# Performance work log

Hardware: AMD Instinct MI355X
Metric: run time of the kernel (lower is better)

The kernel has to match this reference:

```python
import jax, jax.numpy as jnp
import numpy as np

B, S, D, H = 4, 2048, 1024, 16
HD = D // H


def setup_inputs() -> dict:
    key = jax.random.key(0)
    ks = jax.random.split(key, 5)
    scale = 1.0 / np.sqrt(D)
    return {
        "x": jax.random.normal(ks[0], (B, S, D), dtype=jnp.float32),
        "W_q": jax.random.normal(ks[1], (D, D), dtype=jnp.float32) * scale,
        "W_k": jax.random.normal(ks[2], (D, D), dtype=jnp.float32) * scale,
        "W_v": jax.random.normal(ks[3], (D, D), dtype=jnp.float32) * scale,
        "W_o": jax.random.normal(ks[4], (D, D), dtype=jnp.float32) * scale,
    }


def reference(x, W_q, W_k, W_v, W_o):
    b, s, d = x.shape
    # fused QKV projections; reshape to per-head layout [b, s, H, HD]
    q = (x @ W_q).reshape(b, s, H, HD)
    k = (x @ W_k).reshape(b, s, H, HD)
    v = (x @ W_v).reshape(b, s, H, HD)
    # scaled dot-product scores [b, H, s, s]
    scores = jnp.einsum("bqhd,bkhd->bhqk", q, k) / jnp.sqrt(jnp.asarray(HD, x.dtype))
    # causal mask: disallow attending to future positions (j > i)
    causal = jnp.tril(jnp.ones((s, s), dtype=bool))
    scores = jnp.where(causal[None, None], scores, jnp.finfo(x.dtype).min)
    attn = jax.nn.softmax(scores, axis=-1)
    # attention output back to [b, s, d], then output projection (W_o applied as x @ W_o.T)
    out = jnp.einsum("bhqk,bkhd->bqhd", attn, v).reshape(b, s, d)
    return out @ W_o.T
```

## Files before the change

### kernel.cpp

```cpp
#include <hip/hip_runtime.h>
#include <hip/hip_bf16.h>
#include <stdint.h>

#define B_  4
#define S_  2048
#define D_  1024
#define H_  16
#define HD_ 64
#define M_  (B_*S_)

typedef __bf16 bf16_t;
typedef __bf16 bf16x8 __attribute__((ext_vector_type(8)));
typedef __bf16 bf16x4 __attribute__((ext_vector_type(4)));
typedef __bf16 bf16x2 __attribute__((ext_vector_type(2)));
typedef float  f32x4  __attribute__((ext_vector_type(4)));
typedef unsigned int uint2v __attribute__((ext_vector_type(2)));

#define EXP2(x) __builtin_amdgcn_exp2f(x)
#define CS_ 0.18033688011112042f

__global__ void cvt_f32_to_bf16(const float* __restrict__ src, bf16_t* __restrict__ dst, int n) {
  int stride = gridDim.x * blockDim.x * 4;
  for (int i = (blockIdx.x * blockDim.x + threadIdx.x) * 4; i < n; i += stride) {
    float4 v = *(const float4*)(src + i);
    bf16x4 o = { (bf16_t)v.x, (bf16_t)v.y, (bf16_t)v.z, (bf16_t)v.w };
    *(bf16x4*)(dst + i) = o;
  }
}

__global__ void cvt_transpose_w(const float* __restrict__ wq, const float* __restrict__ wk,
                                const float* __restrict__ wv, const float* __restrict__ wof,
                                bf16_t* __restrict__ dst, bf16_t* __restrict__ wob) {
  __shared__ float t[32][33];
  int w = blockIdx.z;
  int c0 = blockIdx.x * 32, r0 = blockIdx.y * 32;
  int tx = threadIdx.x, ty = threadIdx.y;
  if (w == 3) {
#pragma unroll
    for (int i = 0; i < 4; i++)
      wob[(size_t)(r0 + ty + i * 8) * D_ + c0 + tx] =
          (bf16_t)wof[(size_t)(r0 + ty + i * 8) * D_ + c0 + tx];
    return;
  }
  const float* src = (w == 0) ? wq : (w == 1) ? wk : wv;
  const float scl = (w == 0) ? CS_ : 1.0f;
#pragma unroll
  for (int i = 0; i < 4; i++)
    t[ty + i * 8][tx] = src[(size_t)(r0 + ty + i * 8) * D_ + c0 + tx];
  __syncthreads();
#pragma unroll
  for (int i = 0; i < 4; i++)
    dst[(size_t)(w * D_ + c0 + ty + i * 8) * D_ + r0 + tx] = (bf16_t)(t[tx][ty + i * 8] * scl);
}

template <typename OutT>
__global__ void gemm_nt(const bf16_t* __restrict__ A, const bf16_t* __restrict__ Bt,
                        OutT* __restrict__ C, int Mt, int N, int K) {
  __shared__ bf16_t As[128 * 64];
  __shared__ bf16_t Bs[128 * 64];
  const int bn = blockIdx.x, bm = blockIdx.y;
  const int tid = threadIdx.x;
  const int wv = tid >> 6, lane = tid & 63;
  const int wr = wv >> 1, wc = wv & 1;
  const int g = lane >> 4, r16 = lane & 15;
  const int m0 = bm * 128, n0 = bn * 128;

  f32x4 acc[4][4] = {};

  for (int kt = 0; kt < K; kt += 64) {
#pragma unroll
    for (int c = 0; c < 4; c++) {
      int ch = wv * 4 + c;
      int o = ch * 1024 + lane * 16;
      int row = o >> 7;
      int c16 = (o >> 4) & 7;
      const bf16_t* gA = A + (size_t)(m0 + row) * K + kt + ((c16 ^ (row & 7)) * 8);
      __builtin_amdgcn_global_load_lds((const __attribute__((address_space(1))) void*)gA,
          (__attribute__((address_space(3))) void*)((char*)As + ch * 1024), 16, 0, 0);
    }
#pragma unroll
    for (int c = 0; c < 4; c++) {
      int ch = wv * 4 + c;
      int o = ch * 1024 + lane * 16;
      int row = o >> 7;
      int c16 = (o >> 4) & 7;
      const bf16_t* gB = Bt + (size_t)(n0 + row) * K + kt + ((c16 ^ (row & 7)) * 8);
      __builtin_amdgcn_global_load_lds((const __attribute__((address_space(1))) void*)gB,
          (__attribute__((address_space(3))) void*)((char*)Bs + ch * 1024), 16, 0, 0);
    }
    __syncthreads();

#pragma unroll
    for (int kk = 0; kk < 2; kk++) {
      bf16x8 af[4], bfv[4];
#pragma unroll
      for (int i = 0; i < 4; i++) {
        int row = wr * 64 + i * 16 + r16;
        af[i] = *(const bf16x8*)((char*)As + row * 128 + (((kk * 4 + g) ^ (row & 7)) * 16));
      }
#pragma unroll
      for (int j = 0; j < 4; j++) {
        int row = wc * 64 + j * 16 + r16;
        bfv[j] = *(const bf16x8*)((char*)Bs + row * 128 + (((kk * 4 + g) ^ (row & 7)) * 16));
      }
#pragma unroll
      for (int i = 0; i < 4; i++)
#pragma unroll
        for (int j = 0; j < 4; j++)
          acc[i][j] = __builtin_amdgcn_mfma_f32_16x16x32_bf16(af[i], bfv[j], acc[i][j], 0, 0, 0);
    }
    __syncthreads();
  }

#pragma unroll
  for (int i = 0; i < 4; i++)
#pragma unroll
    for (int j = 0; j < 4; j++)
#pragma unroll
      for (int rr = 0; rr < 4; rr++) {
        int grow = m0 + wr * 64 + i * 16 + g * 4 + rr;
        int gcol = n0 + wc * 64 + j * 16 + r16;
        C[(size_t)grow * N + gcol] = (OutT)acc[i][j][rr];
      }
}

__global__ __launch_bounds__(256, 3) void attn_kernel(const bf16_t* __restrict__ QKV,
                                                      bf16_t* __restrict__ AO) {
  const int bh = blockIdx.x;
  const int qt = 31 - (int)blockIdx.y;
  const int b = bh >> 4, h = bh & 15;
  const int tid = threadIdx.x, wv = tid >> 6, lane = tid & 63;
  const int g = lane >> 4, r16 = lane & 15;

  __shared__ bf16_t Ks[2][64 * 64];
  __shared__ bf16_t Vt[2][64 * 64];

  const size_t rowbase = (size_t)b * S_;
  const bf16_t* Qg = QKV + (rowbase + qt * 64) * 3072 + h * HD_;
  const bf16_t* Kg = QKV + rowbase * 3072 + 1024 + h * HD_;
  const bf16_t* Vg = QKV + rowbase * 3072 + 2048 + h * HD_;

  bf16x8 qf0, qf1;
  {
    int row = wv * 16 + r16;
    const bf16_t* p = Qg + (size_t)row * 3072;
    qf0 = *(const bf16x8*)(p + g * 8);
    qf1 = *(const bf16x8*)(p + 32 + g * 8);
  }

  f32x4 o_acc[4] = {};
  float lrow = 0.f;
  const int base_row = qt * 64 + wv * 16;

  const int kp0 = tid >> 4, dq = tid & 15;
  bf16x4 va0, vb0, va1, vb1;

  auto issueK = [&](int t, int buf) {
    const int kv0 = t * 64;
#pragma unroll
    for (int c = 0; c < 2; c++) {
      int chunkid = wv * 2 + c;
      int o = chunkid * 1024 + lane * 16;
      int row = o >> 7;
      int ch = (o >> 4) & 7;
      const bf16_t* src = Kg + (size_t)(kv0 + row) * 3072 + ((ch ^ (row & 7)) * 8);
      __builtin_amdgcn_global_load_lds((const __attribute__((address_space(1))) void*)src,
          (__attribute__((address_space(3))) void*)((char*)(&Ks[buf][0]) + chunkid * 1024), 16, 0, 0);
    }
  };
  auto loadV = [&](int t) {
    const int kv0 = t * 64;
    const bf16_t* p0 = Vg + (size_t)(kv0 + kp0 * 2) * 3072 + dq * 4;
    va0 = *(const bf16x4*)p0;
    vb0 = *(const bf16x4*)(p0 + 3072);
    const bf16_t* p1 = Vg + (size_t)(kv0 + (16 + kp0) * 2) * 3072 + dq * 4;
    va1 = *(const bf16x4*)p1;
    vb1 = *(const bf16x4*)(p1 + 3072);
  };
  auto writeV = [&](int buf) {
#pragma unroll
    for (int j = 0; j < 4; j++) {
      int d = dq * 4 + j;
      int sz = (((d & 7) ^ (d >> 3)) << 2);
      bf16x2 q0 = { va0[j], vb0[j] };
      *(bf16x2*)(&Vt[buf][d * 64 + (kp0 ^ sz) * 2]) = q0;
      bf16x2 q1 = { va1[j], vb1[j] };
      *(bf16x2*)(&Vt[buf][d * 64 + ((16 + kp0) ^ sz) * 2]) = q1;
    }
  };

  issueK(0, 0);
  loadV(0);

  const int ntiles = qt + 1;
  for (int t = 0; t < ntiles; t++) {
    const int cur = t & 1;
    const int kv0 = t * 64;

    asm volatile("s_waitcnt vmcnt(0)" ::: "memory");
    writeV(cur);
    __syncthreads();
    if (t + 1 < ntiles) { issueK(t + 1, cur ^ 1); loadV(t + 1); }

    const bool skip = kv0 > base_row + 15;
    const bool needmask = (kv0 + 63) > base_row;

    f32x4 st[4];
    if (!skip) {
      __builtin_amdgcn_s_setprio(1);
#pragma unroll
      for (int sub = 0; sub < 4; sub++) {
        int krow = sub * 16 + r16;
        bf16x8 k0 = *(const bf16x8*)((char*)(&Ks[cur][0]) + krow * 128 + ((g ^ (krow & 7)) * 16));
        bf16x8 k1 = *(const bf16x8*)((char*)(&Ks[cur][0]) + krow * 128 + (((4 + g) ^ (krow & 7)) * 16));
        if (kv0 + sub * 16 > base_row + 15) {
          f32x4 ninf = { -1e30f, -1e30f, -1e30f, -1e30f };
          st[sub] = ninf;
          continue;
        }
        f32x4 z = {};
        z = __builtin_amdgcn_mfma_f32_16x16x32_bf16(k0, qf0, z, 0, 0, 0);
        z = __builtin_amdgcn_mfma_f32_16x16x32_bf16(k1, qf1, z, 0, 0, 0);
        st[sub] = z;
      }
      __builtin_amdgcn_s_setprio(0);

      const int qrow = base_row + r16;
      if (needmask) {
#pragma unroll
        for (int sub = 0; sub < 4; sub++)
#pragma unroll
          for (int rr = 0; rr < 4; rr++)
            if (kv0 + sub * 16 + g * 4 + rr > qrow) st[sub][rr] = -1e30f;
      }
      float lsum = 0.f;
      unsigned int W[4][2];
#pragma unroll
      for (int sub = 0; sub < 4; sub++)
#pragma unroll
        for (int rrp = 0; rrp < 2; rrp++) {
          float p0 = EXP2(st[sub][2 * rrp]);
          float p1 = EXP2(st[sub][2 * rrp + 1]);
          lsum += p0 + p1;
          bf16x2 pp = { (bf16_t)p0, (bf16_t)p1 };
          W[sub][rrp] = *(unsigned int*)&pp;
        }
      lrow += lsum;
      unsigned int pfw[2][4];
#pragma unroll
      for (int k2 = 0; k2 < 2; k2++)
#pragma unroll
        for (int rrp = 0; rrp < 2; rrp++) {
          uint2v xy = __builtin_amdgcn_permlane32_swap(W[2 * k2][rrp], W[2 * k2 + 1][rrp],
                                                       false, false);
          uint2v zw = __builtin_amdgcn_permlane16_swap(xy[0], xy[1], false, false);
          pfw[k2][rrp]     = zw[0];
          pfw[k2][2 + rrp] = zw[1];
        }
      bf16x8 pf[2];
#pragma unroll
      for (int kh = 0; kh < 2; kh++) {
        union { unsigned int u[4]; bf16x8 v8; } U;
        U.u[0] = pfw[kh][0]; U.u[1] = pfw[kh][1];
        U.u[2] = pfw[kh][2]; U.u[3] = pfw[kh][3];
        pf[kh] = U.v8;
      }

      __builtin_amdgcn_s_setprio(1);
#pragma unroll
      for (int kh = 0; kh < 2; kh++) {
#pragma unroll
        for (int c = 0; c < 4; c++) {
          int d = c * 16 + r16;
          int wstart = (kh * 16 + g * 4) ^ (((d & 7) ^ (d >> 3)) << 2);
          bf16x8 vf = *(const bf16x8*)(&Vt[cur][d * 64 + wstart * 2]);
          o_acc[c] = __builtin_amdgcn_mfma_f32_16x16x32_bf16(vf, pf[kh], o_acc[c], 0, 0, 0);
        }
      }
      __builtin_amdgcn_s_setprio(0);
    }
  }

  {
    float v = lrow;
    v += __shfl_xor(v, 16);
    v += __shfl_xor(v, 32);
    float linv = 1.0f / v;
    const size_t grow = rowbase + base_row + r16;
#pragma unroll
    for (int c = 0; c < 4; c++) {
      bf16x4 o = { (bf16_t)(o_acc[c][0] * linv), (bf16_t)(o_acc[c][1] * linv),
                   (bf16_t)(o_acc[c][2] * linv), (bf16_t)(o_acc[c][3] * linv) };
      *(bf16x4*)(&AO[grow * D_ + h * HD_ + c * 16 + g * 4]) = o;
    }
  }
}

extern "C" void kernel_launch(void* const* d_in, const int* in_sizes, int n_in,
                              void* d_out, int out_size, void* d_ws, size_t ws_size,
                              hipStream_t stream) {
  const float* x  = (const float*)d_in[0];
  const float* Wq = (const float*)d_in[1];
  const float* Wk = (const float*)d_in[2];
  const float* Wv = (const float*)d_in[3];
  const float* Wo = (const float*)d_in[4];
  float* out = (float*)d_out;

  char* ws = (char*)d_ws;
  bf16_t* xb   = (bf16_t*)(ws);
  bf16_t* wqkv = (bf16_t*)(ws + 16777216);
  bf16_t* wo   = (bf16_t*)(ws + 16777216 + 6291456);
  bf16_t* qkv  = (bf16_t*)(ws + 25165824);
  bf16_t* ao   = (bf16_t*)(ws + 75497472);

  cvt_f32_to_bf16<<<1024, 256, 0, stream>>>(x, xb, M_ * D_);
  cvt_transpose_w<<<dim3(32, 32, 4), dim3(32, 8), 0, stream>>>(Wq, Wk, Wv, Wo, wqkv, wo);

  gemm_nt<bf16_t><<<dim3(3072 / 128, M_ / 128), 256, 0, stream>>>(xb, wqkv, qkv, M_, 3072, D_);

  attn_kernel<<<dim3(B_ * H_, 32), 256, 0, stream>>>(qkv, ao);

  gemm_nt<float><<<dim3(D_ / 128, M_ / 128), 256, 0, stream>>>(ao, wo, out, M_, D_, D_);
}
```

Measured before the change: 171.4 us.

## Write V pre-transposed from QKV GEMM epilogue and async-load it in attention

The QKV projection now has its own GEMM kernel whose epilogue writes Q and K to a 2048-wide buffer and V transposed per head into a [b,h,d,token] buffer. The attention kernel then loads V tiles straight into LDS with the same swizzled global_load_lds path used for K, which drops the register-staged transpose and scattered LDS writes done every tile. The cost is moved to the GEMM epilogue, which now does strided 8-byte stores for the V part.

```diff
diff --git a/kernel.cpp b/kernel.cpp
--- a/kernel.cpp
+++ b/kernel.cpp
@@ -124,7 +124,94 @@
       }
 }
 
-__global__ __launch_bounds__(256, 3) void attn_kernel(const bf16_t* __restrict__ QKV,
+__global__ void gemm_qkv(const bf16_t* __restrict__ A, const bf16_t* __restrict__ Bt,
+                         bf16_t* __restrict__ qk, bf16_t* __restrict__ vt) {
+  const int K = D_, N = 3072;
+  __shared__ bf16_t As[128 * 64];
+  __shared__ bf16_t Bs[128 * 64];
+  const int bn = blockIdx.x, bm = blockIdx.y;
+  const int tid = threadIdx.x;
+  const int wv = tid >> 6, lane = tid & 63;
+  const int wr = wv >> 1, wc = wv & 1;
+  const int g = lane >> 4, r16 = lane & 15;
+  const int m0 = bm * 128, n0 = bn * 128;
+
+  f32x4 acc[4][4] = {};
+
+  for (int kt = 0; kt < K; kt += 64) {
+#pragma unroll
+    for (int c = 0; c < 4; c++) {
+      int ch = wv * 4 + c;
+      int o = ch * 1024 + lane * 16;
+      int row = o >> 7;
+      int c16 = (o >> 4) & 7;
+      const bf16_t* gA = A + (size_t)(m0 + row) * K + kt + ((c16 ^ (row & 7)) * 8);
+      __builtin_amdgcn_global_load_lds((const __attribute__((address_space(1))) void*)gA,
+          (__attribute__((address_space(3))) void*)((char*)As + ch * 1024), 16, 0, 0);
+    }
+#pragma unroll
+    for (int c = 0; c < 4; c++) {
+      int ch = wv * 4 + c;
+      int o = ch * 1024 + lane * 16;
+      int row = o >> 7;
+      int c16 = (o >> 4) & 7;
+      const bf16_t* gB = Bt + (size_t)(n0 + row) * K + kt + ((c16 ^ (row & 7)) * 8);
+      __builtin_amdgcn_global_load_lds((const __attribute__((address_space(1))) void*)gB,
+          (__attribute__((address_space(3))) void*)((char*)Bs + ch * 1024), 16, 0, 0);
+    }
+    __syncthreads();
+
+#pragma unroll
+    for (int kk = 0; kk < 2; kk++) {
+      bf16x8 af[4], bfv[4];
+#pragma unroll
+      for (int i = 0; i < 4; i++) {
+        int row = wr * 64 + i * 16 + r16;
+        af[i] = *(const bf16x8*)((char*)As + row * 128 + (((kk * 4 + g) ^ (row & 7)) * 16));
+      }
+#pragma unroll
+      for (int j = 0; j < 4; j++) {
+        int row = wc * 64 + j * 16 + r16;
+        bfv[j] = *(const bf16x8*)((char*)Bs + row * 128 + (((kk * 4 + g) ^ (row & 7)) * 16));
+      }
+#pragma unroll
+      for (int i = 0; i < 4; i++)
+#pragma unroll
+        for (int j = 0; j < 4; j++)
+          acc[i][j] = __builtin_amdgcn_mfma_f32_16x16x32_bf16(af[i], bfv[j], acc[i][j], 0, 0, 0);
+    }
+    __syncthreads();
+  }
+
+  if (n0 < 2048) {
+#pragma unroll
+    for (int i = 0; i < 4; i++)
+#pragma unroll
+      for (int j = 0; j < 4; j++)
+#pragma unroll
+        for (int rr = 0; rr < 4; rr++) {
+          int grow = m0 + wr * 64 + i * 16 + g * 4 + rr;
+          int gcol = n0 + wc * 64 + j * 16 + r16;
+          qk[(size_t)grow * 2048 + gcol] = (bf16_t)acc[i][j][rr];
+        }
+  } else {
+    const int b = m0 >> 11;
+#pragma unroll
+    for (int i = 0; i < 4; i++)
+#pragma unroll
+      for (int j = 0; j < 4; j++) {
+        int dfull = (n0 - 2048) + wc * 64 + j * 16 + r16;
+        int h = dfull >> 6, dd = dfull & 63;
+        int tok = m0 + wr * 64 + i * 16 + g * 4;
+        bf16x4 o = { (bf16_t)acc[i][j][0], (bf16_t)acc[i][j][1],
+                     (bf16_t)acc[i][j][2], (bf16_t)acc[i][j][3] };
+        *(bf16x4*)(&vt[(size_t)((b * 16 + h) * 64 + dd) * 2048 + (tok & 2047)]) = o;
+      }
+  }
+}
+
+__global__ __launch_bounds__(256, 3) void attn_kernel(const bf16_t* __restrict__ qk,
+                                                      const bf16_t* __restrict__ VT,
                                                       bf16_t* __restrict__ AO) {
   const int bh = blockIdx.x;
   const int qt = 31 - (int)blockIdx.y;
@@ -136,14 +223,14 @@
   __shared__ bf16_t Vt[2][64 * 64];
 
   const size_t rowbase = (size_t)b * S_;
-  const bf16_t* Qg = QKV + (rowbase + qt * 64) * 3072 + h * HD_;
-  const bf16_t* Kg = QKV + rowbase * 3072 + 1024 + h * HD_;
-  const bf16_t* Vg = QKV + rowbase * 3072 + 2048 + h * HD_;
+  const bf16_t* Qg = qk + (rowbase + qt * 64) * 2048 + h * HD_;
+  const bf16_t* Kg = qk + rowbase * 2048 + 1024 + h * HD_;
+  const bf16_t* vtb = VT + (size_t)bh * 64 * 2048;
 
   bf16x8 qf0, qf1;
   {
     int row = wv * 16 + r16;
-    const bf16_t* p = Qg + (size_t)row * 3072;
+    const bf16_t* p = Qg + (size_t)row * 2048;
     qf0 = *(const bf16x8*)(p + g * 8);
     qf1 = *(const bf16x8*)(p + 32 + g * 8);
   }
@@ -152,9 +239,6 @@
   float lrow = 0.f;
   const int base_row = qt * 64 + wv * 16;
 
-  const int kp0 = tid >> 4, dq = tid & 15;
-  bf16x4 va0, vb0, va1, vb1;
-
   auto issueK = [&](int t, int buf) {
     const int kv0 = t * 64;
 #pragma unroll
@@ -163,34 +247,27 @@
       int o = chunkid * 1024 + lane * 16;
       int row = o >> 7;
       int ch = (o >> 4) & 7;
-      const bf16_t* src = Kg + (size_t)(kv0 + row) * 3072 + ((ch ^ (row & 7)) * 8);
+      const bf16_t* src = Kg + (size_t)(kv0 + row) * 2048 + ((ch ^ (row & 7)) * 8);
       __builtin_amdgcn_global_load_lds((const __attribute__((address_space(1))) void*)src,
           (__attribute__((address_space(3))) void*)((char*)(&Ks[buf][0]) + chunkid * 1024), 16, 0, 0);
     }
   };
-  auto loadV = [&](int t) {
+  auto issueVt = [&](int t, int buf) {
     const int kv0 = t * 64;
-    const bf16_t* p0 = Vg + (size_t)(kv0 + kp0 * 2) * 3072 + dq * 4;
-    va0 = *(const bf16x4*)p0;
-    vb0 = *(const bf16x4*)(p0 + 3072);
-    const bf16_t* p1 = Vg + (size_t)(kv0 + (16 + kp0) * 2) * 3072 + dq * 4;
-    va1 = *(const bf16x4*)p1;
-    vb1 = *(const bf16x4*)(p1 + 3072);
+#pragma unroll
+    for (int c = 0; c < 2; c++) {
+      int chunkid = wv * 2 + c;
+      int o = chunkid * 1024 + lane * 16;
+      int row = o >> 7;
+      int ch = (o >> 4) & 7;
+      const bf16_t* src = vtb + (size_t)row * 2048 + kv0 + ((ch ^ (row & 7)) * 8);
+      __builtin_amdgcn_global_load_lds((const __attribute__((address_space(1))) void*)src,
+          (__attribute__((address_space(3))) void*)((char*)(&Vt[buf][0]) + chunkid * 1024), 16, 0, 0);
+    }
   };
-  auto writeV = [&](int buf) {
-#pragma unroll
-    for (int j = 0; j < 4; j++) {
-      int d = dq * 4 + j;
-      int sz = (((d & 7) ^ (d >> 3)) << 2);
-      bf16x2 q0 = { va0[j], vb0[j] };
-      *(bf16x2*)(&Vt[buf][d * 64 + (kp0 ^ sz) * 2]) = q0;
-      bf16x2 q1 = { va1[j], vb1[j] };
-      *(bf16x2*)(&Vt[buf][d * 64 + ((16 + kp0) ^ sz) * 2]) = q1;
-    }
-  };
 
   issueK(0, 0);
-  loadV(0);
+  issueVt(0, 0);
 
   const int ntiles = qt + 1;
   for (int t = 0; t < ntiles; t++) {
@@ -198,15 +275,14 @@
     const int kv0 = t * 64;
 
     asm volatile("s_waitcnt vmcnt(0)" ::: "memory");
-    writeV(cur);
     __syncthreads();
-    if (t + 1 < ntiles) { issueK(t + 1, cur ^ 1); loadV(t + 1); }
+    if (t + 1 < ntiles) { issueK(t + 1, cur ^ 1); issueVt(t + 1, cur ^ 1); }
 
     const bool skip = kv0 > base_row + 15;
     const bool needmask = (kv0 + 63) > base_row;
 
-    f32x4 st[4];
     if (!skip) {
+      f32x4 st[4];
       __builtin_amdgcn_s_setprio(1);
 #pragma unroll
       for (int sub = 0; sub < 4; sub++) {
@@ -272,8 +348,7 @@
 #pragma unroll
         for (int c = 0; c < 4; c++) {
           int d = c * 16 + r16;
-          int wstart = (kh * 16 + g * 4) ^ (((d & 7) ^ (d >> 3)) << 2);
-          bf16x8 vf = *(const bf16x8*)(&Vt[cur][d * 64 + wstart * 2]);
+          bf16x8 vf = *(const bf16x8*)((char*)(&Vt[cur][0]) + d * 128 + (((kh * 4 + g) ^ (d & 7)) * 16));
           o_acc[c] = __builtin_amdgcn_mfma_f32_16x16x32_bf16(vf, pf[kh], o_acc[c], 0, 0, 0);
         }
       }
@@ -309,16 +384,17 @@
   char* ws = (char*)d_ws;
   bf16_t* xb   = (bf16_t*)(ws);
   bf16_t* wqkv = (bf16_t*)(ws + 16777216);
-  bf16_t* wo   = (bf16_t*)(ws + 16777216 + 6291456);
-  bf16_t* qkv  = (bf16_t*)(ws + 25165824);
+  bf16_t* wo   = (bf16_t*)(ws + 23068672);
+  bf16_t* qk   = (bf16_t*)(ws + 25165824);
+  bf16_t* vt   = (bf16_t*)(ws + 58720256);
   bf16_t* ao   = (bf16_t*)(ws + 75497472);
 
   cvt_f32_to_bf16<<<1024, 256, 0, stream>>>(x, xb, M_ * D_);
   cvt_transpose_w<<<dim3(32, 32, 4), dim3(32, 8), 0, stream>>>(Wq, Wk, Wv, Wo, wqkv, wo);
 
-  gemm_nt<bf16_t><<<dim3(3072 / 128, M_ / 128), 256, 0, stream>>>(xb, wqkv, qkv, M_, 3072, D_);
-
-  attn_kernel<<<dim3(B_ * H_, 32), 256, 0, stream>>>(qkv, ao);
+  gemm_qkv<<<dim3(3072 / 128, M_ / 128), 256, 0, stream>>>(xb, wqkv, qk, vt);
+
+  attn_kernel<<<dim3(B_ * H_, 32), 256, 0, stream>>>(qk, vt, ao);
 
   gemm_nt<float><<<dim3(D_ / 128, M_ / 128), 256, 0, stream>>>(ao, wo, out, M_, D_, D_);
 }
```

New measurement: 162.3 us. -5.3%, faster.
